# Kernel tuning notes

Hardware: AMD Instinct MI355X
Metric: run time of the kernel (lower is better)

The kernel has to match this reference:

```python
import jax, jax.numpy as jnp
import numpy as np

K = 3
STRIDE = 1
PAD = 1
DIL = 1


def conv2d(x, w, b, stride, pad, dil):
    y = jax.lax.conv_general_dilated(
        x, w, (stride, stride), [(pad, pad), (pad, pad)],
        rhs_dilation=(dil, dil), dimension_numbers=("NCHW", "OIHW", "NCHW"))
    return y + b[None, :, None, None]


def bilinear_gather(img, ys, xs):
    # img: (C,H,W); ys,xs: (KK,Ho,Wo) pixel coords.
    # grid_sample(mode=bilinear, padding_mode=zeros, align_corners=True):
    # out-of-range corners contribute 0, interpolation weights unchanged.
    H, W = img.shape[-2:]
    y0 = jnp.floor(ys)
    x0 = jnp.floor(xs)
    wy1 = ys - y0
    wx1 = xs - x0
    wy0 = 1.0 - wy1
    wx0 = 1.0 - wx1

    def g(yc, xc):
        yi = yc.astype(jnp.int32)
        xi = xc.astype(jnp.int32)
        valid = (yi >= 0) & (yi < H) & (xi >= 0) & (xi < W)
        yi = jnp.clip(yi, 0, H - 1)
        xi = jnp.clip(xi, 0, W - 1)
        v = img[:, yi, xi]  # (C,KK,Ho,Wo)
        return v * valid[None].astype(img.dtype)

    return (g(y0, x0) * (wy0 * wx0)[None]
            + g(y0, x0 + 1.0) * (wy0 * wx1)[None]
            + g(y0 + 1.0, x0) * (wy1 * wx0)[None]
            + g(y0 + 1.0, x0 + 1.0) * (wy1 * wx1)[None])


def setup_inputs() -> dict:
    key = jax.random.key(0)
    ks = jax.random.split(key, 4)
    B, C_in, H, W = 8, 64, 96, 96
    C_out = 64
    x = jax.random.normal(ks[0], (B, C_in, H, W), dtype=jnp.float32)
    weight = jax.random.normal(ks[1], (C_out, C_in, K, K), dtype=jnp.float32) * 0.05
    bias = jax.random.normal(ks[2], (C_out,), dtype=jnp.float32) * 0.01
    off_w = jax.random.normal(ks[3], (2 * K * K, C_in, K, K), dtype=jnp.float32) * 0.05
    off_b = jnp.zeros((2 * K * K,), dtype=jnp.float32)
    return {"x": x, "weight": weight, "bias": bias, "off_w": off_w, "off_b": off_b}


def reference(x, weight, bias, off_w, off_b):
    B, C, H, W = x.shape
    Ho = (H + 2 * PAD - DIL * (K - 1) - 1) // STRIDE + 1
    Wo = (W + 2 * PAD - DIL * (K - 1) - 1) // STRIDE + 1

    offsets = conv2d(x, off_w, off_b, STRIDE, PAD, DIL)  # (B,2*K*K,Ho,Wo)
    off = offsets.reshape(B, K * K, 2, Ho, Wo)

    # Base sampling grid (note: original code does NOT subtract padding; kept faithful).
    by, bx = jnp.meshgrid(jnp.arange(Ho, dtype=x.dtype), jnp.arange(Wo, dtype=x.dtype), indexing="ij")
    by = by * STRIDE + (K // 2) * DIL
    bx = bx * STRIDE + (K // 2) * DIL
    ko = jnp.arange(-(K // 2), K // 2 + 1, dtype=x.dtype)
    ky, kx = jnp.meshgrid(ko, ko, indexing="ij")

    sy = by[None, None] + ky.reshape(1, -1, 1, 1) + off[:, :, 0]  # (B,KK,Ho,Wo)
    sx = bx[None, None] + kx.reshape(1, -1, 1, 1) + off[:, :, 1]

    sampled = jax.vmap(bilinear_gather)(x, sy, sx)  # (B,C,KK,Ho,Wo)

    wflat = weight.reshape(weight.shape[0], C, K * K)  # (O,C,KK)
    out = jnp.einsum("bckhw,ock->bohw", sampled, wflat)
    return out + bias[None, :, None, None]
```

## Files before the change

kernel.cpp:

```cpp
#include <hip/hip_runtime.h>
#include <hip/hip_bf16.h>

#define HH 96
#define WW 96
#define HW 9216
#define NB 8

typedef __bf16 bf16x8 __attribute__((ext_vector_type(8)));
typedef float  f32x4  __attribute__((ext_vector_type(4)));

union BF8 { uint4 u; bf16x8 v; unsigned short s[8]; };

__device__ __forceinline__ unsigned short f2bf_bits(float f) {
    unsigned u = __float_as_uint(f);
    unsigned r = u + 0x7FFFu + ((u >> 16) & 1u);
    return (unsigned short)(r >> 16);
}
__device__ __forceinline__ float bf2f(unsigned short s) {
    return __uint_as_float(((unsigned)s) << 16);
}
__device__ __forceinline__ unsigned pkbf(float a, float b) {
    union { __hip_bfloat162 h; unsigned u; } c;
    c.h = __float22bfloat162_rn(make_float2(a, b));
    return c.u;
}

__device__ __forceinline__ void bl_setup(int h, int w, int r, int s, float oy, float ox,
                                         int* a, float* wg) {
    float sy = (float)(h + r) + oy;
    float sx = (float)(w + s) + ox;
    float fy = floorf(sy), fx = floorf(sx);
    int   y0 = (int)fy, x0 = (int)fx;
    int   y1 = y0 + 1, x1 = x0 + 1;
    float wy1 = sy - fy, wx1 = sx - fx;
    float wy0 = 1.f - wy1, wx0 = 1.f - wx1;
    float m00 = (y0 >= 0 && y0 < HH && x0 >= 0 && x0 < WW) ? 1.f : 0.f;
    float m01 = (y0 >= 0 && y0 < HH && x1 >= 0 && x1 < WW) ? 1.f : 0.f;
    float m10 = (y1 >= 0 && y1 < HH && x0 >= 0 && x0 < WW) ? 1.f : 0.f;
    float m11 = (y1 >= 0 && y1 < HH && x1 >= 0 && x1 < WW) ? 1.f : 0.f;
    int cy0 = min(max(y0, 0), HH - 1), cy1 = min(max(y1, 0), HH - 1);
    int cx0 = min(max(x0, 0), WW - 1), cx1 = min(max(x1, 0), WW - 1);
    a[0] = (cy0 * WW + cx0) * 64;  a[1] = (cy0 * WW + cx1) * 64;
    a[2] = (cy1 * WW + cx0) * 64;  a[3] = (cy1 * WW + cx1) * 64;
    wg[0] = wy0 * wx0 * m00;  wg[1] = wy0 * wx1 * m01;
    wg[2] = wy1 * wx0 * m10;  wg[3] = wy1 * wx1 * m11;
}

__global__ __launch_bounds__(256) void xcvt_prep(const float* __restrict__ x,
                                                 const float* __restrict__ weight,
                                                 const float* __restrict__ off_w,
                                                 unsigned short* __restrict__ xt,
                                                 unsigned short* __restrict__ wTb2,
                                                 unsigned short* __restrict__ owTb2) {
    __shared__ unsigned short T[64 * 64];
    int bid   = blockIdx.x;
    int t     = threadIdx.x;
    int b     = bid & 7;
    int pbase = (bid >> 3) * 64;
    int pl    = t & 63;
    int q     = t >> 6;

    const float* xp = x + ((size_t)(b * 64 + q * 16)) * HW + pbase + pl;
    unsigned short hb[16];
#pragma unroll
    for (int i = 0; i < 16; ++i) hb[i] = f2bf_bits(xp[(size_t)i * HW]);

    uint4 w0, w1;
    w0.x = hb[0]  | (hb[1]  << 16); w0.y = hb[2]  | (hb[3]  << 16);
    w0.z = hb[4]  | (hb[5]  << 16); w0.w = hb[6]  | (hb[7]  << 16);
    w1.x = hb[8]  | (hb[9]  << 16); w1.y = hb[10] | (hb[11] << 16);
    w1.z = hb[12] | (hb[13] << 16); w1.w = hb[14] | (hb[15] << 16);
    int sw = pl & 7;
    *(uint4*)&T[pl * 64 + (((2 * q)     ^ sw) << 3)] = w0;
    *(uint4*)&T[pl * 64 + (((2 * q + 1) ^ sw) << 3)] = w1;
    __syncthreads();

    int row = t >> 2, rs = row & 7;
    uint4 a  = *(const uint4*)&T[row * 64 + ((((t & 3) * 2)     ^ rs) << 3)];
    uint4 b2 = *(const uint4*)&T[row * 64 + ((((t & 3) * 2 + 1) ^ rs) << 3)];
    unsigned short* dst = xt + ((size_t)(b * HW + pbase)) * 64 + t * 16;
    *(uint4*)dst       = a;
    *(uint4*)(dst + 8) = b2;

    if (bid < 216) {
        int i = bid * 256 + t;
        if (i < 36864) {
            int ch = i & 7, lnn = (i >> 3) & 15, qdd = (i >> 7) & 3;
            int kc = (i >> 9) & 1, ct = (i >> 10) & 3, tap = i >> 12;
            int co = ct * 16 + lnn;
            int c  = kc * 32 + qdd * 8 + ch;
            wTb2[i] = f2bf_bits(weight[(co * 64 + c) * 9 + tap]);
        } else {
            int f = i - 36864;
            int ch = f & 7, lnn = (f >> 3) & 15, qdd = (f >> 7) & 3;
            int kc = (f >> 9) & 1, jt = (f >> 10) & 1, tap = f >> 11;
            int j = jt * 16 + lnn;
            int c = kc * 32 + qdd * 8 + ch;
            owTb2[f] = (j < 18) ? f2bf_bits(off_w[(j * 64 + c) * 9 + tap]) : (unsigned short)0;
        }
    }
}

__global__ __launch_bounds__(256, 2) void deform_all(const unsigned short* __restrict__ xt,
                                                     const unsigned short* __restrict__ wTb2,
                                                     const unsigned short* __restrict__ owTb2,
                                                     const float* __restrict__ bias,
                                                     const float* __restrict__ ob,
                                                     float* __restrict__ out) {
    __shared__ float offs[4][16 * 20];

    int bid   = blockIdx.x;
    int t     = threadIdx.x;
    int b     = bid & 7;
    int wv    = t >> 6;
    int l     = t & 63;
    int ln    = l & 15;
    int qd    = l >> 4;
    int pbase = (bid >> 3) * 64 + wv * 16;
    int px    = pbase + ln;
    int h     = px / WW, w = px - h * WW;

    const unsigned short* xb = xt + (size_t)b * HW * 64;

    uint4 pa0[9], pa1[9];
    int   vmsk[9];
#pragma unroll
    for (int tap = 0; tap < 9; ++tap) {
        int  r  = tap / 3, s = tap - r * 3;
        int  iy = h - 1 + r, ix = w - 1 + s;
        vmsk[tap] = ((iy >= 0) & (iy < HH) & (ix >= 0) & (ix < WW)) ? -1 : 0;
        int  rec = (min(max(iy, 0), HH - 1) * WW + min(max(ix, 0), WW - 1)) * 64;
        pa0[tap] = *(const uint4*)(xb + rec + qd * 8);
        pa1[tap] = *(const uint4*)(xb + rec + 32 + qd * 8);
    }
    __builtin_amdgcn_sched_barrier(0);

    f32x4 aj0 = {0.f, 0.f, 0.f, 0.f};
    f32x4 aj1 = {0.f, 0.f, 0.f, 0.f};
#pragma unroll
    for (int tap = 0; tap < 9; ++tap) {
        unsigned m = (unsigned)vmsk[tap];
        BF8 a0, a1;
        a0.u.x = pa0[tap].x & m; a0.u.y = pa0[tap].y & m;
        a0.u.z = pa0[tap].z & m; a0.u.w = pa0[tap].w & m;
        a1.u.x = pa1[tap].x & m; a1.u.y = pa1[tap].y & m;
        a1.u.z = pa1[tap].z & m; a1.u.w = pa1[tap].w & m;

        const unsigned short* base0 = owTb2 + (size_t)tap * 2048 + l * 8;
        BF8 b00, b01, b10, b11;
        b00.u = *(const uint4*)(base0);
        b01.u = *(const uint4*)(base0 + 512);
        b10.u = *(const uint4*)(base0 + 1024);
        b11.u = *(const uint4*)(base0 + 1536);
        aj0 = __builtin_amdgcn_mfma_f32_16x16x32_bf16(a0.v, b00.v, aj0, 0, 0, 0);
        aj0 = __builtin_amdgcn_mfma_f32_16x16x32_bf16(a1.v, b01.v, aj0, 0, 0, 0);
        aj1 = __builtin_amdgcn_mfma_f32_16x16x32_bf16(a0.v, b10.v, aj1, 0, 0, 0);
        aj1 = __builtin_amdgcn_mfma_f32_16x16x32_bf16(a1.v, b11.v, aj1, 0, 0, 0);
    }

    {
        float* ow_ = offs[wv];
        float  obj = ob[ln];
#pragma unroll
        for (int rg = 0; rg < 4; ++rg) ow_[(qd * 4 + rg) * 20 + ln] = aj0[rg] + obj;
        if (ln < 2) {
            float obj1 = ob[16 + ln];
#pragma unroll
            for (int rg = 0; rg < 4; ++rg) ow_[(qd * 4 + rg) * 20 + 16 + ln] = aj1[rg] + obj1;
        }
    }
    float oy[9], ox[9];
#pragma unroll
    for (int k = 0; k < 9; ++k) {
        float2 p = *(const float2*)&offs[wv][ln * 20 + 2 * k];
        oy[k] = p.x; ox[k] = p.y;
    }

    f32x4 acc[4] = {{0.f,0.f,0.f,0.f},{0.f,0.f,0.f,0.f},{0.f,0.f,0.f,0.f},{0.f,0.f,0.f,0.f}};

    uint4 cf0[2][4], cf1[2][4];
    float gs[2][4];

    {
        int a_[4];
        bl_setup(h, w, 0, 0, oy[0], ox[0], a_, gs[0]);
#pragma unroll
        for (int c = 0; c < 4; ++c) {
            cf0[0][c] = *(const uint4*)(xb + a_[c] + qd * 8);
            cf1[0][c] = *(const uint4*)(xb + a_[c] + 32 + qd * 8);
        }
        bl_setup(h, w, 0, 1, oy[1], ox[1], a_, gs[1]);
#pragma unroll
        for (int c = 0; c < 4; ++c) {
            cf0[1][c] = *(const uint4*)(xb + a_[c] + qd * 8);
            cf1[1][c] = *(const uint4*)(xb + a_[c] + 32 + qd * 8);
        }
    }
    __builtin_amdgcn_sched_barrier(0);

#pragma unroll
    for (int k = 0; k < 9; ++k) {
        int slot = k & 1;

        BF8 A0, A1;
        {
            BF8 q0, q1, q2, q3, r0, r1, r2, r3;
            q0.u = cf0[slot][0]; q1.u = cf0[slot][1]; q2.u = cf0[slot][2]; q3.u = cf0[slot][3];
            r0.u = cf1[slot][0]; r1.u = cf1[slot][1]; r2.u = cf1[slot][2]; r3.u = cf1[slot][3];
            float g0 = gs[slot][0], g1 = gs[slot][1], g2 = gs[slot][2], g3 = gs[slot][3];
            float v0[8], v1[8];
#pragma unroll
            for (int i = 0; i < 8; ++i) {
                v0[i] = g0 * bf2f(q0.s[i]) + g1 * bf2f(q1.s[i])
                      + g2 * bf2f(q2.s[i]) + g3 * bf2f(q3.s[i]);
                v1[i] = g0 * bf2f(r0.s[i]) + g1 * bf2f(r1.s[i])
                      + g2 * bf2f(r2.s[i]) + g3 * bf2f(r3.s[i]);
            }
            A0.u.x = pkbf(v0[0], v0[1]); A0.u.y = pkbf(v0[2], v0[3]);
            A0.u.z = pkbf(v0[4], v0[5]); A0.u.w = pkbf(v0[6], v0[7]);
            A1.u.x = pkbf(v1[0], v1[1]); A1.u.y = pkbf(v1[2], v1[3]);
            A1.u.z = pkbf(v1[4], v1[5]); A1.u.w = pkbf(v1[6], v1[7]);
        }

        if (k + 2 < 9) {
            int kk = k + 2;
            int r = kk / 3, s = kk - r * 3;
            int a_[4];
            bl_setup(h, w, r, s, oy[kk], ox[kk], a_, gs[slot]);
#pragma unroll
            for (int c = 0; c < 4; ++c) {
                cf0[slot][c] = *(const uint4*)(xb + a_[c] + qd * 8);
                cf1[slot][c] = *(const uint4*)(xb + a_[c] + 32 + qd * 8);
            }
        }

        const unsigned short* wb = wTb2 + (size_t)k * 4096 + l * 8;
#pragma unroll
        for (int ct = 0; ct < 4; ++ct) {
            BF8 B0, B1;
            B0.u = *(const uint4*)(wb + ct * 1024);
            B1.u = *(const uint4*)(wb + ct * 1024 + 512);
            acc[ct] = __builtin_amdgcn_mfma_f32_16x16x32_bf16(A0.v, B0.v, acc[ct], 0, 0, 0);
            acc[ct] = __builtin_amdgcn_mfma_f32_16x16x32_bf16(A1.v, B1.v, acc[ct], 0, 0, 0);
        }

        __builtin_amdgcn_sched_barrier(0);
    }

#pragma unroll
    for (int ct = 0; ct < 4; ++ct) {
        int   co = ct * 16 + ln;
        float bv = bias[co];
        float4 st;
        st.x = acc[ct][0] + bv; st.y = acc[ct][1] + bv;
        st.z = acc[ct][2] + bv; st.w = acc[ct][3] + bv;
        *(float4*)(out + ((size_t)(b * 64 + co)) * HW + pbase + qd * 4) = st;
    }
}

extern "C" void kernel_launch(void* const* d_in, const int* in_sizes, int n_in,
                              void* d_out, int out_size, void* d_ws, size_t ws_size,
                              hipStream_t stream) {
    const float* x      = (const float*)d_in[0];
    const float* weight = (const float*)d_in[1];
    const float* bias   = (const float*)d_in[2];
    const float* off_w  = (const float*)d_in[3];
    const float* off_b  = (const float*)d_in[4];
    float* out = (float*)d_out;

    unsigned short* xt    = (unsigned short*)d_ws;
    unsigned short* wTb2  = xt + 4718592;
    unsigned short* owTb2 = wTb2 + 36864;

    hipLaunchKernelGGL(xcvt_prep,  dim3(1152), dim3(256), 0, stream,
                       x, weight, off_w, xt, wTb2, owTb2);
    hipLaunchKernelGGL(deform_all, dim3(1152), dim3(256), 0, stream,
                       xt, wTb2, owTb2, bias, off_b, out);
}
```

Measured before the change: 147.7 us.

## Stage main conv weights in LDS and double-buffer offset-conv weight loads

Each block copies the full bf16 main-conv weight tensor (72 KB) into shared memory once, and the main MFMA loop then reads B fragments from LDS instead of global memory. The offset-conv weight fragments are now prefetched two taps ahead in registers. The goal is to hide global-load latency for the weight operands. The cost is a large LDS allocation that may limit occupancy below the two blocks per CU requested by the launch bounds, a per-block prologue copy plus __syncthreads, and extra register pressure.

```diff
diff --git a/kernel.cpp b/kernel.cpp
--- a/kernel.cpp
+++ b/kernel.cpp
@@ -107,6 +107,7 @@
                                                      const float* __restrict__ bias,
                                                      const float* __restrict__ ob,
                                                      float* __restrict__ out) {
+    __shared__ unsigned short Wlds[36864];
     __shared__ float offs[4][16 * 20];
 
     int bid   = blockIdx.x;
@@ -122,6 +123,14 @@
 
     const unsigned short* xb = xt + (size_t)b * HW * 64;
 
+    {
+        const uint4* src = (const uint4*)wTb2;
+        uint4*       dst = (uint4*)Wlds;
+#pragma unroll
+        for (int i = 0; i < 18; ++i) dst[i * 256 + t] = src[i * 256 + t];
+    }
+    __syncthreads();
+
     uint4 pa0[9], pa1[9];
     int   vmsk[9];
 #pragma unroll
@@ -133,29 +142,44 @@
         pa0[tap] = *(const uint4*)(xb + rec + qd * 8);
         pa1[tap] = *(const uint4*)(xb + rec + 32 + qd * 8);
     }
+    uint4 obf[2][4];
+#pragma unroll
+    for (int p = 0; p < 2; ++p) {
+        const unsigned short* base0 = owTb2 + (size_t)p * 2048 + l * 8;
+        obf[p][0] = *(const uint4*)(base0);
+        obf[p][1] = *(const uint4*)(base0 + 512);
+        obf[p][2] = *(const uint4*)(base0 + 1024);
+        obf[p][3] = *(const uint4*)(base0 + 1536);
+    }
     __builtin_amdgcn_sched_barrier(0);
 
     f32x4 aj0 = {0.f, 0.f, 0.f, 0.f};
     f32x4 aj1 = {0.f, 0.f, 0.f, 0.f};
 #pragma unroll
     for (int tap = 0; tap < 9; ++tap) {
+        int slot = tap & 1;
         unsigned m = (unsigned)vmsk[tap];
-        BF8 a0, a1;
+        BF8 a0, a1, b00, b01, b10, b11;
         a0.u.x = pa0[tap].x & m; a0.u.y = pa0[tap].y & m;
         a0.u.z = pa0[tap].z & m; a0.u.w = pa0[tap].w & m;
         a1.u.x = pa1[tap].x & m; a1.u.y = pa1[tap].y & m;
         a1.u.z = pa1[tap].z & m; a1.u.w = pa1[tap].w & m;
-
-        const unsigned short* base0 = owTb2 + (size_t)tap * 2048 + l * 8;
-        BF8 b00, b01, b10, b11;
-        b00.u = *(const uint4*)(base0);
-        b01.u = *(const uint4*)(base0 + 512);
-        b10.u = *(const uint4*)(base0 + 1024);
-        b11.u = *(const uint4*)(base0 + 1536);
+        b00.u = obf[slot][0]; b01.u = obf[slot][1];
+        b10.u = obf[slot][2]; b11.u = obf[slot][3];
+
+        if (tap + 2 < 9) {
+            const unsigned short* base0 = owTb2 + (size_t)(tap + 2) * 2048 + l * 8;
+            obf[slot][0] = *(const uint4*)(base0);
+            obf[slot][1] = *(const uint4*)(base0 + 512);
+            obf[slot][2] = *(const uint4*)(base0 + 1024);
+            obf[slot][3] = *(const uint4*)(base0 + 1536);
+        }
+
         aj0 = __builtin_amdgcn_mfma_f32_16x16x32_bf16(a0.v, b00.v, aj0, 0, 0, 0);
         aj0 = __builtin_amdgcn_mfma_f32_16x16x32_bf16(a1.v, b01.v, aj0, 0, 0, 0);
         aj1 = __builtin_amdgcn_mfma_f32_16x16x32_bf16(a0.v, b10.v, aj1, 0, 0, 0);
         aj1 = __builtin_amdgcn_mfma_f32_16x16x32_bf16(a1.v, b11.v, aj1, 0, 0, 0);
+        __builtin_amdgcn_sched_barrier(0);
     }
 
     {
@@ -201,6 +225,13 @@
 #pragma unroll
     for (int k = 0; k < 9; ++k) {
         int slot = k & 1;
+
+        BF8 B0[4], B1[4];
+#pragma unroll
+        for (int ct = 0; ct < 4; ++ct) {
+            B0[ct].u = *(const uint4*)&Wlds[k * 4096 + ct * 1024 + l * 8];
+            B1[ct].u = *(const uint4*)&Wlds[k * 4096 + ct * 1024 + 512 + l * 8];
+        }
 
         BF8 A0, A1;
         {
@@ -234,14 +265,10 @@
             }
         }
 
-        const unsigned short* wb = wTb2 + (size_t)k * 4096 + l * 8;
 #pragma unroll
         for (int ct = 0; ct < 4; ++ct) {
-            BF8 B0, B1;
-            B0.u = *(const uint4*)(wb + ct * 1024);
-            B1.u = *(const uint4*)(wb + ct * 1024 + 512);
-            acc[ct] = __builtin_amdgcn_mfma_f32_16x16x32_bf16(A0.v, B0.v, acc[ct], 0, 0, 0);
-            acc[ct] = __builtin_amdgcn_mfma_f32_16x16x32_bf16(A1.v, B1.v, acc[ct], 0, 0, 0);
+            acc[ct] = __builtin_amdgcn_mfma_f32_16x16x32_bf16(A0.v, B0[ct].v, acc[ct], 0, 0, 0);
+            acc[ct] = __builtin_amdgcn_mfma_f32_16x16x32_bf16(A1.v, B1[ct].v, acc[ct], 0, 0, 0);
         }
 
         __builtin_amdgcn_sched_barrier(0);
```

New measurement: 140.2 us. 5.1% less time.
